# Optimization experiments

Measured on AMD Instinct MI355X. Metric: run time of the kernel, lower is better.

The kernel has to match this reference:

```python
import jax, jax.numpy as jnp
import numpy as np

EPSILON = 0.3
ALPHA = 0.7
LN_EPS = 1e-5


def _layernorm(x, g, b):
    mu = jnp.mean(x, axis=-1, keepdims=True)
    var = jnp.mean((x - mu) ** 2, axis=-1, keepdims=True)
    return (x - mu) / jnp.sqrt(var + LN_EPS) * g + b


def setup_inputs() -> dict:
    key = jax.random.key(0)
    ks = jax.random.split(key, 6)
    B, N, D, L = 1, 2048, 768, 16
    s = 0.05  # weight scale to keep sigmoid/exp well-conditioned
    return {
        "x": jax.random.normal(ks[0], (B, N, D), jnp.float32),
        "proj_w": jax.random.normal(ks[1], (D, L), jnp.float32) * s,
        "proj_b": jnp.zeros((L,), jnp.float32),
        "ln1_g": jnp.ones((L,), jnp.float32),
        "ln1_b": jnp.zeros((L,), jnp.float32),
        "pi_w1": jax.random.normal(ks[2], (L, D), jnp.float32) * s,
        "pi_b1": jnp.zeros((D,), jnp.float32),
        "pi_w2": jax.random.normal(ks[3], (D, 1), jnp.float32) * s,
        "pi_b2": jnp.zeros((1,), jnp.float32),
        "dt": jnp.full((1,), 0.05, jnp.float32),
        "f_w": jax.random.normal(ks[4], (D, D), jnp.float32) * s,
        "f_b": jnp.zeros((D,), jnp.float32),
        "ln2_g": jnp.ones((D,), jnp.float32),
        "ln2_b": jnp.zeros((D,), jnp.float32),
    }


def reference(x, proj_w, proj_b, ln1_g, ln1_b, pi_w1, pi_b1, pi_w2, pi_b2, dt, f_w, f_b, ln2_g, ln2_b):
    B, N, D = x.shape
    # proj_list: Linear -> LayerNorm -> ReLU. [B,N,L]
    x_proj = jax.nn.relu(_layernorm(x @ proj_w + proj_b, ln1_g, ln1_b))
    # RBF kernel over pairwise differences. [B,N,N]
    diff = x_proj[:, :, None, :] - x_proj[:, None, :, :]
    K_eps = jnp.exp(-(1.0 / (4.0 * EPSILON)) * jnp.sum(diff * diff, axis=-1))
    q_tilde = jnp.sum(K_eps, axis=2)  # [B,N]
    # pi_list: Linear -> ReLU -> Linear -> Sigmoid. [B,N]
    pi = jax.nn.sigmoid(jax.nn.relu(x_proj @ pi_w1 + pi_b1) @ pi_w2 + pi_b2)[..., 0]
    v = pi / q_tilde  # diagonal of D_epsilon_tilde
    # K_tilde = K_eps @ diag(v): column scaling (math-equivalent to bmm with diag_embed)
    K_tilde = K_eps * v[:, None, :]
    d = jnp.sum(K_tilde, axis=2) + 1e-5  # diagonal of D_tilde
    # inv(D_tilde) @ K_tilde: row scaling; then subtract identity
    L_op = (1.0 / EPSILON) * (K_tilde / d[:, :, None]) - jnp.eye(N, dtype=x.dtype)[None]
    L_mat = L_op[0]  # .squeeze(0), B == 1
    # f(x): modeled as linear map
    target = x @ f_w + f_b  # [B,N,D]
    tt = dt * jnp.einsum('ij,bjd->bid', L_mat, target)  # target_transformed
    target1 = target + tt
    target2 = ALPHA * x + (1.0 - ALPHA) * (target1 + tt)
    return _layernorm(target2, ln2_g, ln2_b)
```

## Files before the change

### kernel.cpp

```cpp
#include <hip/hip_runtime.h>
#include <math.h>

#define EPSILON 0.3f
#define ALPHA 0.7f
#define LN_EPS 1e-5f

typedef __bf16 bf16x8 __attribute__((ext_vector_type(8)));
typedef float f32x4 __attribute__((ext_vector_type(4)));

__device__ __forceinline__ unsigned short f2bf(float f) {
  unsigned int u = __float_as_uint(f);
  return (unsigned short)((u + 0x7fffu + ((u >> 16) & 1u)) >> 16);
}
__device__ __forceinline__ unsigned int pack2(float lo, float hi) {
  return (unsigned int)f2bf(lo) | ((unsigned int)f2bf(hi) << 16);
}

__device__ __forceinline__ void async16(const unsigned short* g,
                                        unsigned short* l) {
  __builtin_amdgcn_global_load_lds(
      (const __attribute__((address_space(1))) unsigned int*)g,
      (__attribute__((address_space(3))) unsigned int*)l, 16, 0, 0);
}

__device__ __forceinline__ float wave_reduce(float v) {
#pragma unroll
  for (int off = 32; off > 0; off >>= 1) v += __shfl_xor(v, off, 64);
  return v;
}

__device__ __forceinline__ float blk_reduce_sum(float v, float* red) {
  v = wave_reduce(v);
  int lane = threadIdx.x & 63, wid = threadIdx.x >> 6;
  __syncthreads();
  if (lane == 0) red[wid] = v;
  __syncthreads();
  return red[0] + red[1] + red[2] + red[3];
}

__global__ __launch_bounds__(256) void k_proj(
    const float* __restrict__ x, const float* __restrict__ proj_w,
    const float* __restrict__ proj_b, const float* __restrict__ ln1_g,
    const float* __restrict__ ln1_b, const float* __restrict__ pi_w1,
    const float* __restrict__ pi_b1, const float* __restrict__ pi_w2,
    const float* __restrict__ pi_b2, const float* __restrict__ fw,
    unsigned short* __restrict__ fwTb, float* __restrict__ xp,
    float* __restrict__ s, float* __restrict__ pi, int N, int D) {
  __shared__ float xs[16][68];
  __shared__ float ws[64][20];
  __shared__ float ysh[16][17];
  __shared__ float xps[16][16];
  __shared__ float pr[16][4];
  int tid = threadIdx.x;
  int nProj = N / 16;
  if (blockIdx.x >= (unsigned)nProj) {
    unsigned short(*tile)[33] = (unsigned short(*)[33])&ws[0][0];
    int t = blockIdx.x - nProj;
    int tx = tid & 31, ty = tid >> 5;
    int cols = D / 32;
    int c0 = (t % cols) * 32, r0 = (t / cols) * 32;
#pragma unroll
    for (int i = 0; i < 4; ++i) {
      int r = r0 + ty + i * 8;
      tile[ty + i * 8][tx] = f2bf(fw[(size_t)r * D + c0 + tx]);
    }
    __syncthreads();
#pragma unroll
    for (int i = 0; i < 4; ++i) {
      int cc = c0 + ty + i * 8;
      fwTb[(size_t)cc * D + r0 + tx] = tile[tx][ty + i * 8];
    }
    return;
  }
  int row0 = blockIdx.x * 16;
  int row = tid >> 4, l = tid & 15;
  int lane = tid & 63, w = tid >> 6;
  int skc = (tid & 15) * 4;
  int wk = tid >> 2, wl = (tid & 3) * 4;
  float acc = 0.f;
  for (int k0 = 0; k0 < D; k0 += 64) {
    float4 xv = *(const float4*)(x + (size_t)(row0 + row) * D + k0 + skc);
    float4 wv = *(const float4*)(proj_w + (size_t)(k0 + wk) * 16 + wl);
    __syncthreads();
    *(float4*)&xs[row][skc] = xv;
    *(float4*)&ws[wk][wl] = wv;
    __syncthreads();
#pragma unroll
    for (int kk = 0; kk < 64; kk += 4) {
      float4 a4 = *(const float4*)&xs[row][kk];
      acc += a4.x * ws[kk + 0][l];
      acc += a4.y * ws[kk + 1][l];
      acc += a4.z * ws[kk + 2][l];
      acc += a4.w * ws[kk + 3][l];
    }
  }
  float y = acc + proj_b[l];
  ysh[row][l] = y;
  __syncthreads();
  float mu = 0.f;
#pragma unroll
  for (int t = 0; t < 16; ++t) mu += ysh[row][t];
  mu *= (1.f / 16.f);
  float var = 0.f;
#pragma unroll
  for (int t = 0; t < 16; ++t) { float d2 = ysh[row][t] - mu; var += d2 * d2; }
  var *= (1.f / 16.f);
  float rstd = rsqrtf(var + LN_EPS);
  float xpv = fmaxf((y - mu) * rstd * ln1_g[l] + ln1_b[l], 0.f);
  xps[row][l] = xpv;
  xp[(size_t)(row0 + row) * 16 + l] = xpv;
  float sq = xpv * xpv;
  sq += __shfl_xor(sq, 8, 64);
  sq += __shfl_xor(sq, 4, 64);
  sq += __shfl_xor(sq, 2, 64);
  sq += __shfl_xor(sq, 1, 64);
  if ((lane & 15) == 0) s[row0 + row] = sq;
  __syncthreads();
  float w1r[3][16], b1r[3], w2r[3];
#pragma unroll
  for (int c = 0; c < 3; ++c) {
    int d0 = tid + c * 256;
    b1r[c] = pi_b1[d0];
    w2r[c] = pi_w2[d0];
#pragma unroll
    for (int t = 0; t < 16; ++t) w1r[c][t] = pi_w1[(size_t)t * D + d0];
  }
#pragma unroll
  for (int r = 0; r < 16; ++r) {
    float xv[16];
#pragma unroll
    for (int t4 = 0; t4 < 4; ++t4) {
      float4 xq = *(const float4*)&xps[r][t4 * 4];
      xv[t4 * 4 + 0] = xq.x; xv[t4 * 4 + 1] = xq.y;
      xv[t4 * 4 + 2] = xq.z; xv[t4 * 4 + 3] = xq.w;
    }
    float pa = 0.f;
#pragma unroll
    for (int c = 0; c < 3; ++c) {
      float h = b1r[c];
#pragma unroll
      for (int t = 0; t < 16; ++t) h += xv[t] * w1r[c][t];
      h = fmaxf(h, 0.f);
      pa += h * w2r[c];
    }
    float pv = wave_reduce(pa);
    if (lane == 0) pr[r][w] = pv;
  }
  __syncthreads();
  if (tid < 16) {
    float tot = pr[tid][0] + pr[tid][1] + pr[tid][2] + pr[tid][3] + pi_b2[0];
    pi[row0 + tid] = 1.f / (1.f + expf(-tot));
  }
}

__global__ __launch_bounds__(256) void k_keps(
    const float* __restrict__ xp, const float* __restrict__ s,
    const float* __restrict__ pi, unsigned short* __restrict__ Kb,
    float* __restrict__ v, int N) {
  __shared__ float qs[4][4];
  int i0 = blockIdx.x * 4;
  int tid = threadIdx.x, lane = tid & 63, w = tid >> 6;
  float a[4][16], si[4];
#pragma unroll
  for (int r = 0; r < 4; ++r) {
    const float* ap = xp + (size_t)(i0 + r) * 16;
#pragma unroll
    for (int t = 0; t < 16; ++t) a[r][t] = ap[t];
    si[r] = s[i0 + r];
  }
  const float c = 1.f / (4.f * EPSILON);
  float qa[4] = {0.f, 0.f, 0.f, 0.f};
  for (int it = 0; it < N / 512; ++it) {
    int j = it * 512 + tid * 2;
    const float4* bp = (const float4*)(xp + (size_t)j * 16);
    float4 b0 = bp[0], b1 = bp[1], b2 = bp[2], b3 = bp[3];
    float4 c0 = bp[4], c1 = bp[5], c2 = bp[6], c3 = bp[7];
    float bv[16] = {b0.x, b0.y, b0.z, b0.w, b1.x, b1.y, b1.z, b1.w,
                    b2.x, b2.y, b2.z, b2.w, b3.x, b3.y, b3.z, b3.w};
    float cv[16] = {c0.x, c0.y, c0.z, c0.w, c1.x, c1.y, c1.z, c1.w,
                    c2.x, c2.y, c2.z, c2.w, c3.x, c3.y, c3.z, c3.w};
    float sj0 = s[j], sj1 = s[j + 1];
#pragma unroll
    for (int r = 0; r < 4; ++r) {
      float d0 = 0.f, d1 = 0.f;
#pragma unroll
      for (int t = 0; t < 16; ++t) { d0 += a[r][t] * bv[t]; d1 += a[r][t] * cv[t]; }
      float k0 = __expf(-c * (si[r] + sj0 - 2.f * d0));
      float k1 = __expf(-c * (si[r] + sj1 - 2.f * d1));
      *(unsigned int*)(Kb + (size_t)(i0 + r) * N + j) = pack2(k0, k1);
      qa[r] += k0 + k1;
    }
  }
#pragma unroll
  for (int r = 0; r < 4; ++r) {
    float t = wave_reduce(qa[r]);
    if (lane == 0) qs[r][w] = t;
  }
  __syncthreads();
  if (tid < 4) {
    float tot = qs[tid][0] + qs[tid][1] + qs[tid][2] + qs[tid][3];
    v[i0 + tid] = pi[i0 + tid] / tot;
  }
}

__global__ __launch_bounds__(256) void k_prep(
    const unsigned short* __restrict__ Kb, const float* __restrict__ v,
    float* __restrict__ dv, const float* __restrict__ x,
    unsigned short* __restrict__ xvbT, int N, int D) {
  __shared__ float sh[544];
  int bid = blockIdx.x, tid = threadIdx.x;
  if (bid < N) {
    int i = bid;
    float acc = 0.f;
    for (int j8 = tid * 8; j8 < N; j8 += 256 * 8) {
      uint4 kv4 = *(const uint4*)(Kb + (size_t)i * N + j8);
      float4 va = *(const float4*)(v + j8);
      float4 vb = *(const float4*)(v + j8 + 4);
      unsigned int u;
      u = kv4.x;
      acc += __uint_as_float(u << 16) * va.x + __uint_as_float(u & 0xffff0000u) * va.y;
      u = kv4.y;
      acc += __uint_as_float(u << 16) * va.z + __uint_as_float(u & 0xffff0000u) * va.w;
      u = kv4.z;
      acc += __uint_as_float(u << 16) * vb.x + __uint_as_float(u & 0xffff0000u) * vb.y;
      u = kv4.w;
      acc += __uint_as_float(u << 16) * vb.z + __uint_as_float(u & 0xffff0000u) * vb.w;
    }
    float tot = blk_reduce_sum(acc, sh);
    if (tid == 0) dv[i] = tot + 1e-5f;
  } else {
    int t = bid - N;
    unsigned short(*tile)[33] = (unsigned short(*)[33])sh;
    int tx = tid & 31, ty = tid >> 5;
    int cols = D / 32;
    int c0 = (t % cols) * 32;
    int r0 = (t / cols) * 32;
#pragma unroll
    for (int i = 0; i < 4; ++i) {
      int r = r0 + ty + i * 8;
      tile[ty + i * 8][tx] = f2bf(v[r] * x[(size_t)r * D + c0 + tx]);
    }
    __syncthreads();
#pragma unroll
    for (int i = 0; i < 4; ++i) {
      int cc = c0 + ty + i * 8;
      xvbT[(size_t)cc * N + r0 + tx] = tile[tx][ty + i * 8];
    }
  }
}

#define GEMM_KLOOP(Aptr, Bptr, Kdim)                                          \
  int tid = threadIdx.x;                                                      \
  int w = tid >> 6, l = tid & 63;                                             \
  int ln = l & 15, quad = l >> 4;                                             \
  int mh = (w & 1) * 32, nh = (w >> 1) * 32;                                  \
  int row0 = blockIdx.y * 64, col0 = blockIdx.x * 64;                         \
  int srow = w * 4 + (l >> 4);                                                \
  int swz = ((l & 15) ^ srow) * 8;                                            \
  const unsigned short* gA = Aptr + (size_t)(row0 + srow) * Kdim + swz;       \
  const unsigned short* gB = Bptr + (size_t)(col0 + srow) * Kdim + swz;       \
  f32x4 acc[2][2] = {};                                                       \
  for (int k0 = 0; k0 < Kdim; k0 += 128) {                                    \
    __syncthreads();                                                          \
    _Pragma("unroll")                                                         \
    for (int q = 0; q < 4; ++q) {                                             \
      async16(gA + (size_t)q * 16 * Kdim + k0, As + (q * 16 + w * 4) * 128);  \
      async16(gB + (size_t)q * 16 * Kdim + k0, Bs + (q * 16 + w * 4) * 128);  \
    }                                                                         \
    __syncthreads();                                                          \
    _Pragma("unroll")                                                         \
    for (int ks = 0; ks < 4; ++ks) {                                          \
      bf16x8 bfr[2], afr[2];                                                  \
      _Pragma("unroll")                                                       \
      for (int nt = 0; nt < 2; ++nt) {                                        \
        int r = nh + nt * 16 + ln;                                            \
        int cix = (ks * 4 + quad) ^ (r & 15);                                 \
        bfr[nt] = *(const bf16x8*)&Bs[r * 128 + cix * 8];                     \
      }                                                                       \
      _Pragma("unroll")                                                       \
      for (int mt = 0; mt < 2; ++mt) {                                        \
        int r = mh + mt * 16 + ln;                                            \
        int cix = (ks * 4 + quad) ^ (r & 15);                                 \
        afr[mt] = *(const bf16x8*)&As[r * 128 + cix * 8];                     \
      }                                                                       \
      _Pragma("unroll")                                                       \
      for (int mt = 0; mt < 2; ++mt)                                          \
        _Pragma("unroll")                                                     \
        for (int nt = 0; nt < 2; ++nt)                                        \
          acc[mt][nt] = __builtin_amdgcn_mfma_f32_16x16x32_bf16(              \
              afr[mt], bfr[nt], acc[mt][nt], 0, 0, 0);                        \
    }                                                                         \
  }

__global__ __launch_bounds__(256) void k_gemmA(
    const unsigned short* __restrict__ A, const unsigned short* __restrict__ Bt,
    const float* __restrict__ x, const float* __restrict__ dv,
    const float* __restrict__ dtp, unsigned short* __restrict__ Z,
    int M, int N, int K) {
  __shared__ unsigned short As[64 * 128];
  __shared__ unsigned short Bs[64 * 128];
  GEMM_KLOOP(A, Bt, K)
  float dtv = dtp[0];
  float c2 = (1.f - ALPHA) * (1.f - 2.f * dtv);
  float c3b = (1.f - ALPHA) * 2.f * dtv / EPSILON;
#pragma unroll
  for (int mt = 0; mt < 2; ++mt)
#pragma unroll
    for (int nt = 0; nt < 2; ++nt) {
      int col = col0 + nh + nt * 16 + ln;
#pragma unroll
      for (int r = 0; r < 4; ++r) {
        int row = row0 + mh + mt * 16 + quad * 4 + r;
        float c3 = c3b / dv[row];
        Z[(size_t)row * N + col] =
            f2bf(c2 * x[(size_t)row * N + col] + c3 * acc[mt][nt][r]);
      }
    }
}

__global__ __launch_bounds__(256) void k_gemmB(
    const unsigned short* __restrict__ A, const unsigned short* __restrict__ Bt,
    const float* __restrict__ x, const float* __restrict__ bias,
    const float* __restrict__ dtp, float* __restrict__ out,
    int M, int N, int K) {
  __shared__ unsigned short As[64 * 128];
  __shared__ unsigned short Bs[64 * 128];
  GEMM_KLOOP(A, Bt, K)
  float dtv = dtp[0];
  float cb = (1.f - ALPHA) * (1.f - 2.f * dtv) +
             (1.f - ALPHA) * 2.f * dtv / EPSILON;
#pragma unroll
  for (int mt = 0; mt < 2; ++mt)
#pragma unroll
    for (int nt = 0; nt < 2; ++nt) {
      int col = col0 + nh + nt * 16 + ln;
      float bv = cb * bias[col];
#pragma unroll
      for (int r = 0; r < 4; ++r) {
        int row = row0 + mh + mt * 16 + quad * 4 + r;
        size_t idx = (size_t)row * N + col;
        out[idx] = ALPHA * x[idx] + acc[mt][nt][r] + bv;
      }
    }
}

__global__ __launch_bounds__(256) void k_ln_rows(
    float* __restrict__ out, const float* __restrict__ g,
    const float* __restrict__ b, int D) {
  __shared__ float red[4];
  int i = blockIdx.x, tid = threadIdx.x;
  float vv[4];
  int nt = D / 256;
  float sum = 0.f;
  for (int t = 0; t < nt; ++t) {
    vv[t] = out[(size_t)i * D + tid + t * 256];
    sum += vv[t];
  }
  float mu = blk_reduce_sum(sum, red) / (float)D;
  float sq = 0.f;
  for (int t = 0; t < nt; ++t) { float d2 = vv[t] - mu; sq += d2 * d2; }
  float var = blk_reduce_sum(sq, red) / (float)D;
  float rs = rsqrtf(var + LN_EPS);
  for (int t = 0; t < nt; ++t) {
    int d0 = tid + t * 256;
    out[(size_t)i * D + d0] = (vv[t] - mu) * rs * g[d0] + b[d0];
  }
}

extern "C" void kernel_launch(void* const* d_in, const int* in_sizes, int n_in,
                              void* d_out, int out_size, void* d_ws, size_t ws_size,
                              hipStream_t stream) {
  const float* x = (const float*)d_in[0];
  const float* proj_w = (const float*)d_in[1];
  const float* proj_b = (const float*)d_in[2];
  const float* ln1_g = (const float*)d_in[3];
  const float* ln1_b = (const float*)d_in[4];
  const float* pi_w1 = (const float*)d_in[5];
  const float* pi_b1 = (const float*)d_in[6];
  const float* pi_w2 = (const float*)d_in[7];
  const float* pi_b2 = (const float*)d_in[8];
  const float* dt = (const float*)d_in[9];
  const float* f_w = (const float*)d_in[10];
  const float* f_b = (const float*)d_in[11];
  const float* ln2_g = (const float*)d_in[12];
  const float* ln2_b = (const float*)d_in[13];
  float* out = (float*)d_out;

  int D = in_sizes[11];
  int N = in_sizes[0] / D;

  unsigned short* Kb = (unsigned short*)d_ws;
  unsigned short* xvbT = Kb + (size_t)N * N;
  unsigned short* fwTb = xvbT + (size_t)D * N;
  unsigned short* Z = fwTb + (size_t)D * D;
  float* xp = (float*)(Z + (size_t)N * D);
  float* s = xp + (size_t)N * 16;
  float* pi = s + N;
  float* v = pi + N;
  float* dv = v + N;

  int fwB = (D / 32) * (D / 32);
  int xvtB = (D / 32) * (N / 32);

  k_proj<<<N / 16 + fwB, 256, 0, stream>>>(x, proj_w, proj_b, ln1_g, ln1_b,
                                           pi_w1, pi_b1, pi_w2, pi_b2, f_w,
                                           fwTb, xp, s, pi, N, D);
  k_keps<<<N / 4, 256, 0, stream>>>(xp, s, pi, Kb, v, N);
  k_prep<<<N + xvtB, 256, 0, stream>>>(Kb, v, dv, x, xvbT, N, D);
  k_gemmA<<<dim3(D / 64, N / 64), 256, 0, stream>>>(Kb, xvbT, x, dv, dt, Z,
                                                    N, D, N);
  k_gemmB<<<dim3(D / 64, N / 64), 256, 0, stream>>>(Z, fwTb, x, f_b, dt, out,
                                                    N, D, D);
  k_ln_rows<<<N, 256, 0, stream>>>(out, ln2_g, ln2_b, D);
}
```

Baseline: 157.9 us.

## Fuse final LayerNorm into second GEMM via last-block-per-row-strip counter

The separate row LayerNorm kernel is removed. Each GEMM-B block bumps an atomic counter for its 64-row strip, and the last block to finish that strip normalizes all 64 rows with one wave per row. A memset clears the counters before the pipeline runs. This saves one kernel launch and a separate pass over the output, but the LayerNorm tail now runs on only one block per strip, and it hardcodes D=768 and relies on wave_reduce and w already existing.

```diff
diff --git a/kernel.cpp b/kernel.cpp
--- a/kernel.cpp
+++ b/kernel.cpp
@@ -318,13 +318,15 @@
     }
 }
 
-__global__ __launch_bounds__(256) void k_gemmB(
+__global__ __launch_bounds__(256) void k_gemmB_ln(
     const unsigned short* __restrict__ A, const unsigned short* __restrict__ Bt,
     const float* __restrict__ x, const float* __restrict__ bias,
-    const float* __restrict__ dtp, float* __restrict__ out,
-    int M, int N, int K) {
+    const float* __restrict__ dtp, const float* __restrict__ g,
+    const float* __restrict__ b, unsigned* __restrict__ cnt,
+    float* __restrict__ out, int M, int N, int K) {
   __shared__ unsigned short As[64 * 128];
   __shared__ unsigned short Bs[64 * 128];
+  __shared__ unsigned done;
   GEMM_KLOOP(A, Bt, K)
   float dtv = dtp[0];
   float cb = (1.f - ALPHA) * (1.f - 2.f * dtv) +
@@ -342,28 +344,48 @@
         out[idx] = ALPHA * x[idx] + acc[mt][nt][r] + bv;
       }
     }
-}
-
-__global__ __launch_bounds__(256) void k_ln_rows(
-    float* __restrict__ out, const float* __restrict__ g,
-    const float* __restrict__ b, int D) {
-  __shared__ float red[4];
-  int i = blockIdx.x, tid = threadIdx.x;
-  float vv[4];
-  int nt = D / 256;
-  float sum = 0.f;
-  for (int t = 0; t < nt; ++t) {
-    vv[t] = out[(size_t)i * D + tid + t * 256];
-    sum += vv[t];
-  }
-  float mu = blk_reduce_sum(sum, red) / (float)D;
-  float sq = 0.f;
-  for (int t = 0; t < nt; ++t) { float d2 = vv[t] - mu; sq += d2 * d2; }
-  float var = blk_reduce_sum(sq, red) / (float)D;
-  float rs = rsqrtf(var + LN_EPS);
-  for (int t = 0; t < nt; ++t) {
-    int d0 = tid + t * 256;
-    out[(size_t)i * D + d0] = (vv[t] - mu) * rs * g[d0] + b[d0];
+  __threadfence();
+  if (tid == 0) done = atomicAdd(cnt + blockIdx.y, 1u);
+  __syncthreads();
+  if (done != gridDim.x - 1) return;
+  __threadfence();
+  int lane = tid & 63;
+  for (int r = w; r < 64; r += 4) {
+    float* rowp = out + (size_t)(row0 + r) * N;
+    float4 a = ((const float4*)rowp)[lane];
+    float4 bq = ((const float4*)rowp)[lane + 64];
+    float4 cq = ((const float4*)rowp)[lane + 128];
+    float sum = a.x + a.y + a.z + a.w + bq.x + bq.y + bq.z + bq.w +
+                cq.x + cq.y + cq.z + cq.w;
+    float mu = wave_reduce(sum) * (1.f / 768.f);
+    float sq = (a.x - mu) * (a.x - mu) + (a.y - mu) * (a.y - mu) +
+               (a.z - mu) * (a.z - mu) + (a.w - mu) * (a.w - mu) +
+               (bq.x - mu) * (bq.x - mu) + (bq.y - mu) * (bq.y - mu) +
+               (bq.z - mu) * (bq.z - mu) + (bq.w - mu) * (bq.w - mu) +
+               (cq.x - mu) * (cq.x - mu) + (cq.y - mu) * (cq.y - mu) +
+               (cq.z - mu) * (cq.z - mu) + (cq.w - mu) * (cq.w - mu);
+    float var = wave_reduce(sq) * (1.f / 768.f);
+    float rs = rsqrtf(var + LN_EPS);
+    float4 g0 = ((const float4*)g)[lane], g1 = ((const float4*)g)[lane + 64],
+           g2 = ((const float4*)g)[lane + 128];
+    float4 b0 = ((const float4*)b)[lane], b1 = ((const float4*)b)[lane + 64],
+           b2 = ((const float4*)b)[lane + 128];
+    float4 o0, o1, o2;
+    o0.x = (a.x - mu) * rs * g0.x + b0.x;
+    o0.y = (a.y - mu) * rs * g0.y + b0.y;
+    o0.z = (a.z - mu) * rs * g0.z + b0.z;
+    o0.w = (a.w - mu) * rs * g0.w + b0.w;
+    o1.x = (bq.x - mu) * rs * g1.x + b1.x;
+    o1.y = (bq.y - mu) * rs * g1.y + b1.y;
+    o1.z = (bq.z - mu) * rs * g1.z + b1.z;
+    o1.w = (bq.w - mu) * rs * g1.w + b1.w;
+    o2.x = (cq.x - mu) * rs * g2.x + b2.x;
+    o2.y = (cq.y - mu) * rs * g2.y + b2.y;
+    o2.z = (cq.z - mu) * rs * g2.z + b2.z;
+    o2.w = (cq.w - mu) * rs * g2.w + b2.w;
+    ((float4*)rowp)[lane] = o0;
+    ((float4*)rowp)[lane + 64] = o1;
+    ((float4*)rowp)[lane + 128] = o2;
   }
 }
 
@@ -398,10 +420,12 @@
   float* pi = s + N;
   float* v = pi + N;
   float* dv = v + N;
+  unsigned* cnt = (unsigned*)(dv + N);
 
   int fwB = (D / 32) * (D / 32);
   int xvtB = (D / 32) * (N / 32);
 
+  hipMemsetAsync(cnt, 0, (N / 64) * sizeof(unsigned), stream);
   k_proj<<<N / 16 + fwB, 256, 0, stream>>>(x, proj_w, proj_b, ln1_g, ln1_b,
                                            pi_w1, pi_b1, pi_w2, pi_b2, f_w,
                                            fwTb, xp, s, pi, N, D);
@@ -409,7 +433,6 @@
   k_prep<<<N + xvtB, 256, 0, stream>>>(Kb, v, dv, x, xvbT, N, D);
   k_gemmA<<<dim3(D / 64, N / 64), 256, 0, stream>>>(Kb, xvbT, x, dv, dt, Z,
                                                     N, D, N);
-  k_gemmB<<<dim3(D / 64, N / 64), 256, 0, stream>>>(Z, fwTb, x, f_b, dt, out,
-                                                    N, D, D);
-  k_ln_rows<<<N, 256, 0, stream>>>(out, ln2_g, ln2_b, D);
-}
+  k_gemmB_ln<<<dim3(D / 64, N / 64), 256, 0, stream>>>(
+      Z, fwTb, x, f_b, dt, ln2_g, ln2_b, cnt, out, N, D, D);
+}
```

New measurement: 225.5 us. +42.9%, slower.
